# Kernel tuning notes

Hardware: AMD Instinct MI355X
Metric: run time of the kernel (lower is better)

## Reference

```python
import jax, jax.numpy as jnp
import numpy as np

S = 0.1  # smoothing constant from __init__
EPS = 1e-08


def setup_inputs() -> dict:
    key = jax.random.key(0)
    am = jax.random.uniform(key, (64, 16, 65536), dtype=jnp.float32)
    return {"am": am}


def reference(am):
    B, K, N = am.shape
    # normalize each slot mask over pixels
    an = am / (jnp.sum(am, axis=-1, keepdims=True) + EPS)  # [B,K,N]
    sums = jnp.sum(an, axis=-1)  # [B,K]
    # pairwise intersections as one batched Gram matmul instead of K*(K-1)/2 tiny reductions
    gram = jnp.einsum('bkn,bln->bkl', an, an)  # [B,K,K]
    union = sums[:, :, None] + sums[:, None, :]  # [B,K,K]
    dice = (2.0 * gram + S) / (union + S)  # [B,K,K]
    per_pair = jnp.mean(dice, axis=0)  # [K,K], mean over batch per pair
    upper = jnp.triu(jnp.ones((K, K), dtype=bool), k=1)  # i < j pairs
    c = K * (K - 1) // 2
    total = jnp.sum(jnp.where(upper, per_pair, 0.0))
    return total / max(c, 1)
```

## Files before the change

### kernel.cpp

```cpp
#include <hip/hip_runtime.h>

#define B_ 64
#define K_ 16
#define N_ 65536
#define CHUNKS 16
#define CW (N_ / CHUNKS)
#define KB_PER_WAVE (CW / 32 / 4)
#define U_ 4
#define REC 320
#define NPAIR 120
#define EPS_ 1e-8f
#define SMOOTH_ 0.1f

typedef __attribute__((ext_vector_type(8))) short bf16x8;
typedef __attribute__((ext_vector_type(4))) float f32x4;

__device__ __forceinline__ short f2bf(float f) {
    unsigned u = __float_as_uint(f);
    return (short)((u + 0x7FFFu + ((u >> 16) & 1u)) >> 16);
}

template <int CTRL>
__device__ __forceinline__ float dpp_add_step(float x) {
    int y = __builtin_amdgcn_update_dpp(0, __float_as_int(x), CTRL, 0xf, 0xf, true);
    return x + __int_as_float(y);
}
__device__ __forceinline__ float wave_sum_lane63(float x) {
    x = dpp_add_step<0x111>(x);
    x = dpp_add_step<0x112>(x);
    x = dpp_add_step<0x114>(x);
    x = dpp_add_step<0x118>(x);
    x = dpp_add_step<0x142>(x);
    x = dpp_add_step<0x143>(x);
    return x;
}

__global__ __launch_bounds__(256, 4)
void dice_accum(const float* __restrict__ am, float* __restrict__ ws) {
    const int b     = blockIdx.x >> 4;
    const int chunk = blockIdx.x & (CHUNKS - 1);
    const int tid   = threadIdx.x;
    const int lane  = tid & 63;
    const int w     = tid >> 6;
    const int row   = lane & 15;
    const int lg    = lane >> 4;

    const float4* __restrict__ rp =
        reinterpret_cast<const float4*>(am)
        + (size_t)(b * K_ + row) * (N_ / 4)
        + chunk * (CW / 4)
        + lg * 2;

    const int rot = (b + chunk * 5 + w * 8) & (KB_PER_WAVE - 1);

    f32x4 acc = {0.f, 0.f, 0.f, 0.f};
    float rs = 0.f;

#pragma unroll 1
    for (int i = 0; i < KB_PER_WAVE; i += U_) {
        float4 a[U_][2];
#pragma unroll
        for (int u = 0; u < U_; ++u) {
            const int kb = w + 4 * ((i + u + rot) & (KB_PER_WAVE - 1));
            a[u][0] = rp[kb * 8];
            a[u][1] = rp[kb * 8 + 1];
        }
#pragma unroll
        for (int u = 0; u < U_; ++u) {
            const float f0 = a[u][0].x, f1 = a[u][0].y, f2 = a[u][0].z, f3 = a[u][0].w;
            const float f4 = a[u][1].x, f5 = a[u][1].y, f6 = a[u][1].z, f7 = a[u][1].w;
            rs += ((f0 + f1) + (f2 + f3)) + ((f4 + f5) + (f6 + f7));
            bf16x8 frag;
            frag[0] = f2bf(f0); frag[1] = f2bf(f1);
            frag[2] = f2bf(f2); frag[3] = f2bf(f3);
            frag[4] = f2bf(f4); frag[5] = f2bf(f5);
            frag[6] = f2bf(f6); frag[7] = f2bf(f7);
            acc = __builtin_amdgcn_mfma_f32_16x16x32_bf16(frag, frag, acc, 0, 0, 0);
        }
    }

    float* __restrict__ rec = ws + ((size_t)blockIdx.x * 4 + w) * REC;
#pragma unroll
    for (int j = 0; j < 4; ++j) {
        const int rrow = lg * 4 + j;
        rec[rrow * 16 + row] = acc[j];
    }
    rec[256 + lane] = rs;
}

__global__ __launch_bounds__(256)
void dice_finalize1(const float* __restrict__ ws, float* __restrict__ ws2) {
    const int b   = blockIdx.x;
    const int tid = threadIdx.x;
    __shared__ float G[256];
    __shared__ float RS[64];
    __shared__ float red[128];

    const float* __restrict__ base = ws + (size_t)b * CHUNKS * 4 * REC;

    float g = 0.f;
#pragma unroll 4
    for (int r = 0; r < CHUNKS * 4; ++r) g += base[r * REC + tid];
    G[tid] = g;

    if (tid < 64) {
        float s = 0.f;
#pragma unroll 4
        for (int r = 0; r < CHUNKS * 4; ++r) s += base[r * REC + 256 + tid];
        RS[tid] = s;
    }
    __syncthreads();
    if (tid < 16) RS[tid] = RS[tid] + RS[tid + 16] + RS[tid + 32] + RS[tid + 48];
    __syncthreads();

    float acc = 0.f;
    if (tid < NPAIR) {
        int rem = tid, k = 0;
        while (rem >= K_ - 1 - k) { rem -= K_ - 1 - k; ++k; }
        const int l = k + 1 + rem;
        const float rsk = RS[k], rsl = RS[l];
        const float dk = rsk + EPS_, dl = rsl + EPS_;
        const float gram = G[k * 16 + l] / (dk * dl);
        const float u    = rsk / dk + rsl / dl;
        acc = (2.f * gram + SMOOTH_) / (u + SMOOTH_);
    }
    if (tid < 128) red[tid] = acc;
    __syncthreads();
    if (tid < 64) {
        float t = red[tid] + red[tid + 64];
        t = wave_sum_lane63(t);
        if (tid == 63) ws2[b] = t;
    }
}

__global__ void dice_finalize2(const float* __restrict__ ws2, float* __restrict__ out) {
    float v = ws2[threadIdx.x];
    v = wave_sum_lane63(v);
    if (threadIdx.x == 63) out[0] = v / (float)(B_ * NPAIR);
}

extern "C" void kernel_launch(void* const* d_in, const int* in_sizes, int n_in,
                              void* d_out, int out_size, void* d_ws, size_t ws_size,
                              hipStream_t stream) {
    const float* am = (const float*)d_in[0];
    float* ws  = (float*)d_ws;
    float* ws2 = ws + (size_t)B_ * CHUNKS * 4 * REC;
    float* out = (float*)d_out;

    hipLaunchKernelGGL(dice_accum, dim3(B_ * CHUNKS), dim3(256), 0, stream, am, ws);
    hipLaunchKernelGGL(dice_finalize1, dim3(B_), dim3(256), 0, stream, ws, ws2);
    hipLaunchKernelGGL(dice_finalize2, dim3(1), dim3(64), 0, stream, ws2, out);
}
```

Baseline: 55.98 us.

## Double-buffer loads, reduce waves in LDS, merge finalize kernels via atomics

The accumulation loop now uses explicit double-buffered nontemporal loads, so the next group's global reads are in flight while the current group's MFMAs run. Each block first combines its four waves' Gram and row-sum partials in LDS and writes one record instead of four, shrinking the workspace traffic. The two finalize kernels become one, which sums the per-batch results with float atomics plus a completion counter, saving a launch. The counter is reset inside the first kernel, which relies on stream ordering, and the float atomic sum is no longer deterministic in order.

```diff
diff --git a/kernel.cpp b/kernel.cpp
--- a/kernel.cpp
+++ b/kernel.cpp
@@ -7,13 +7,16 @@
 #define CW (N_ / CHUNKS)
 #define KB_PER_WAVE (CW / 32 / 4)
 #define U_ 4
-#define REC 320
+#define NGRP (KB_PER_WAVE / U_)
+#define REC 272
 #define NPAIR 120
 #define EPS_ 1e-8f
 #define SMOOTH_ 0.1f
 
 typedef __attribute__((ext_vector_type(8))) short bf16x8;
 typedef __attribute__((ext_vector_type(4))) float f32x4;
+
+#define WS_REC_OFF 16
 
 __device__ __forceinline__ short f2bf(float f) {
     unsigned u = __float_as_uint(f);
@@ -45,72 +48,103 @@
     const int row   = lane & 15;
     const int lg    = lane >> 4;
 
-    const float4* __restrict__ rp =
-        reinterpret_cast<const float4*>(am)
+    if (blockIdx.x == 0 && tid == 0) {
+        reinterpret_cast<unsigned*>(ws)[0] = 0u;
+        ws[1] = 0.f;
+    }
+
+    const f32x4* __restrict__ rp =
+        reinterpret_cast<const f32x4*>(am)
         + (size_t)(b * K_ + row) * (N_ / 4)
         + chunk * (CW / 4)
         + lg * 2;
 
     const int rot = (b + chunk * 5 + w * 8) & (KB_PER_WAVE - 1);
 
-    f32x4 acc = {0.f, 0.f, 0.f, 0.f};
+    typedef __attribute__((ext_vector_type(4))) float accv;
+    accv acc = {0.f, 0.f, 0.f, 0.f};
     float rs = 0.f;
 
+    f32x4 aA[U_][2], aB[U_][2];
+
+#define LOADG(dst, g) { _Pragma("unroll")                                     \
+    for (int u = 0; u < U_; ++u) {                                            \
+        const int kb = w + 4 * (((g) * U_ + u + rot) & (KB_PER_WAVE - 1));    \
+        dst[u][0] = __builtin_nontemporal_load(&rp[kb * 8]);                  \
+        dst[u][1] = __builtin_nontemporal_load(&rp[kb * 8 + 1]); } }
+
+#define COMP(src) { _Pragma("unroll")                                         \
+    for (int u = 0; u < U_; ++u) {                                            \
+        const float f0 = src[u][0].x, f1 = src[u][0].y,                       \
+                    f2 = src[u][0].z, f3 = src[u][0].w;                       \
+        const float f4 = src[u][1].x, f5 = src[u][1].y,                       \
+                    f6 = src[u][1].z, f7 = src[u][1].w;                       \
+        rs += ((f0 + f1) + (f2 + f3)) + ((f4 + f5) + (f6 + f7));              \
+        bf16x8 frag;                                                          \
+        frag[0] = f2bf(f0); frag[1] = f2bf(f1);                               \
+        frag[2] = f2bf(f2); frag[3] = f2bf(f3);                               \
+        frag[4] = f2bf(f4); frag[5] = f2bf(f5);                               \
+        frag[6] = f2bf(f6); frag[7] = f2bf(f7);                               \
+        acc = __builtin_amdgcn_mfma_f32_16x16x32_bf16(frag, frag, acc, 0, 0, 0); } }
+
+    LOADG(aA, 0)
 #pragma unroll 1
-    for (int i = 0; i < KB_PER_WAVE; i += U_) {
-        float4 a[U_][2];
+    for (int g = 0; g < NGRP - 2; g += 2) {
+        LOADG(aB, g + 1)
+        COMP(aA)
+        LOADG(aA, g + 2)
+        COMP(aB)
+    }
+    LOADG(aB, NGRP - 1)
+    COMP(aA)
+    COMP(aB)
+#undef LOADG
+#undef COMP
+
+    __shared__ float G_lds[4][256];
+    __shared__ float RS_lds[4][64];
 #pragma unroll
-        for (int u = 0; u < U_; ++u) {
-            const int kb = w + 4 * ((i + u + rot) & (KB_PER_WAVE - 1));
-            a[u][0] = rp[kb * 8];
-            a[u][1] = rp[kb * 8 + 1];
-        }
+    for (int j = 0; j < 4; ++j)
+        G_lds[w][(lg * 4 + j) * 16 + row] = acc[j];
+    RS_lds[w][lane] = rs;
+    __syncthreads();
+
+    float* __restrict__ rec = ws + WS_REC_OFF + (size_t)blockIdx.x * REC;
+    {
+        float g = G_lds[0][tid] + G_lds[1][tid] + G_lds[2][tid] + G_lds[3][tid];
+        rec[tid] = g;
+    }
+    if (tid < 16) {
+        float s = 0.f;
 #pragma unroll
-        for (int u = 0; u < U_; ++u) {
-            const float f0 = a[u][0].x, f1 = a[u][0].y, f2 = a[u][0].z, f3 = a[u][0].w;
-            const float f4 = a[u][1].x, f5 = a[u][1].y, f6 = a[u][1].z, f7 = a[u][1].w;
-            rs += ((f0 + f1) + (f2 + f3)) + ((f4 + f5) + (f6 + f7));
-            bf16x8 frag;
-            frag[0] = f2bf(f0); frag[1] = f2bf(f1);
-            frag[2] = f2bf(f2); frag[3] = f2bf(f3);
-            frag[4] = f2bf(f4); frag[5] = f2bf(f5);
-            frag[6] = f2bf(f6); frag[7] = f2bf(f7);
-            acc = __builtin_amdgcn_mfma_f32_16x16x32_bf16(frag, frag, acc, 0, 0, 0);
-        }
+        for (int ww = 0; ww < 4; ++ww)
+#pragma unroll
+            for (int g2 = 0; g2 < 4; ++g2) s += RS_lds[ww][g2 * 16 + tid];
+        rec[256 + tid] = s;
     }
-
-    float* __restrict__ rec = ws + ((size_t)blockIdx.x * 4 + w) * REC;
-#pragma unroll
-    for (int j = 0; j < 4; ++j) {
-        const int rrow = lg * 4 + j;
-        rec[rrow * 16 + row] = acc[j];
-    }
-    rec[256 + lane] = rs;
 }
 
 __global__ __launch_bounds__(256)
-void dice_finalize1(const float* __restrict__ ws, float* __restrict__ ws2) {
+void dice_finalize(float* __restrict__ ws, float* __restrict__ out) {
     const int b   = blockIdx.x;
     const int tid = threadIdx.x;
     __shared__ float G[256];
-    __shared__ float RS[64];
+    __shared__ float RS[16];
     __shared__ float red[128];
+    __shared__ float bpart;
 
-    const float* __restrict__ base = ws + (size_t)b * CHUNKS * 4 * REC;
+    const float* __restrict__ base = ws + WS_REC_OFF + (size_t)b * CHUNKS * REC;
 
     float g = 0.f;
-#pragma unroll 4
-    for (int r = 0; r < CHUNKS * 4; ++r) g += base[r * REC + tid];
+#pragma unroll
+    for (int r = 0; r < CHUNKS; ++r) g += base[r * REC + tid];
     G[tid] = g;
-
-    if (tid < 64) {
+    if (tid < 16) {
         float s = 0.f;
-#pragma unroll 4
-        for (int r = 0; r < CHUNKS * 4; ++r) s += base[r * REC + 256 + tid];
+#pragma unroll
+        for (int r = 0; r < CHUNKS; ++r) s += base[r * REC + 256 + tid];
         RS[tid] = s;
     }
-    __syncthreads();
-    if (tid < 16) RS[tid] = RS[tid] + RS[tid + 16] + RS[tid + 32] + RS[tid + 48];
     __syncthreads();
 
     float acc = 0.f;
@@ -129,14 +163,21 @@
     if (tid < 64) {
         float t = red[tid] + red[tid + 64];
         t = wave_sum_lane63(t);
-        if (tid == 63) ws2[b] = t;
+        if (tid == 63) bpart = t;
     }
-}
+    __syncthreads();
 
-__global__ void dice_finalize2(const float* __restrict__ ws2, float* __restrict__ out) {
-    float v = ws2[threadIdx.x];
-    v = wave_sum_lane63(v);
-    if (threadIdx.x == 63) out[0] = v / (float)(B_ * NPAIR);
+    if (tid == 0) {
+        atomicAdd(&ws[1], bpart);
+        __threadfence();
+        unsigned old = atomicAdd(reinterpret_cast<unsigned*>(ws), 1u);
+        if (old == B_ - 1) {
+            __threadfence();
+            float total = __hip_atomic_load(&ws[1], __ATOMIC_RELAXED,
+                                            __HIP_MEMORY_SCOPE_AGENT);
+            out[0] = total / (float)(B_ * NPAIR);
+        }
+    }
 }
 
 extern "C" void kernel_launch(void* const* d_in, const int* in_sizes, int n_in,
@@ -144,10 +185,8 @@
                               hipStream_t stream) {
     const float* am = (const float*)d_in[0];
     float* ws  = (float*)d_ws;
-    float* ws2 = ws + (size_t)B_ * CHUNKS * 4 * REC;
     float* out = (float*)d_out;
 
     hipLaunchKernelGGL(dice_accum, dim3(B_ * CHUNKS), dim3(256), 0, stream, am, ws);
-    hipLaunchKernelGGL(dice_finalize1, dim3(B_), dim3(256), 0, stream, ws, ws2);
-    hipLaunchKernelGGL(dice_finalize2, dim3(1), dim3(64), 0, stream, ws2, out);
+    hipLaunchKernelGGL(dice_finalize, dim3(B_), dim3(256), 0, stream, ws, out);
 }
```

Result: no change. 56.81 us (+1.5%).
